# Performance work log

Measured on AMD Instinct MI355X. Metric: run time of the kernel, lower is better.

The kernel has to match this reference:

```python
import jax, jax.numpy as jnp
import numpy as np

_WINDOW = 2  # len_sort_window in the torch module


def _butterfly_indices(L, D):
    """Replicates get_butterfly_matrix's index columns.

    Column 0 is arange(L). Each subsequent column d (1-indexed) is arange(L)
    rolled right by shift_offset, where shift_offset starts at 0 and increases
    by 2 per column (mod L). The butterfly_factor_to_matrix result is computed
    but never used in the original code, so it is omitted here.
    Result[i, d] = (i - shift_d) mod L.
    """
    shifts = np.concatenate([[0], (_WINDOW * np.arange(D - 1)) % L])  # [D]
    idx = (np.arange(L)[:, None] - shifts[None, :]) % L  # [L, D]
    return jnp.asarray(idx, dtype=jnp.int32)


def setup_inputs() -> dict:
    key = jax.random.key(0)
    v = jax.random.normal(key, (16, 16384, 128), dtype=jnp.float32)
    return {"v": v}


def reference(v):
    B, L, D = v.shape  # static under jit
    idx = _butterfly_indices(L, D)  # [L, D]
    # v_shifted[b, i, d] = v[b, idx[i, d], d]  (torch.gather along dim 1)
    v_shifted = jnp.take_along_axis(v, jnp.broadcast_to(idx[None], (B, L, D)), axis=1)
    # window-2 ascending sort == compare-exchange (min, max)
    vw = v_shifted.reshape(B, L // _WINDOW, _WINDOW, D)
    lo = jnp.minimum(vw[:, :, 0], vw[:, :, 1])
    hi = jnp.maximum(vw[:, :, 0], vw[:, :, 1])
    out = jnp.stack([lo, hi], axis=2).reshape(B, L, D)
    return out
```

## Files before the change

kernel.cpp:

```cpp
#include <hip/hip_runtime.h>
#include <cstdint>
#include <cstddef>

#define L_DIM 16384
#define D_DIM 128
#define B_DIM 16

#define TR 256
#define DG 32
#define HALO 64
#define ROWS (TR + HALO)

__global__ __launch_bounds__(256) void butterfly_cmpex_kernel(
    const float* __restrict__ v, float* __restrict__ out) {
  __shared__ float lds[ROWS * DG];

  const int rtile = blockIdx.x;
  const int g     = blockIdx.y;
  const int b     = blockIdx.z;
  const int r0    = rtile * TR;
  const int d0    = g * DG;
  const int smax  = 64 * g + 60;
  const int rin0  = r0 - smax;

  const int t    = threadIdx.x;
  const int lane = t & 63;
  const int wave = t >> 6;

  const float* vb = v + (size_t)b * L_DIM * D_DIM;

  const int lrow  = lane >> 3;
  const int lcol4 = lane & 7;
  for (int chunk = wave; chunk < ROWS / 8; chunk += 4) {
    const int grow = (rin0 + chunk * 8 + lrow) & (L_DIM - 1);
    const float* gp = vb + (size_t)grow * D_DIM + d0 + lcol4 * 4;
    float* lp = &lds[chunk * 8 * DG];
    __builtin_amdgcn_global_load_lds(
        (const __attribute__((address_space(1))) uint32_t*)gp,
        (__attribute__((address_space(3))) uint32_t*)lp,
        16 , 0 , 0 );
  }
  __syncthreads();

  const int c  = t & 31;
  const int jg = t >> 5;
  const int d  = d0 + c;
  const int s  = (d == 0) ? 0 : (2 * d - 2);
  const int roff = smax - s;

  float* outb = out + (size_t)b * L_DIM * D_DIM;

#pragma unroll
  for (int k = 0; k < TR / 16; ++k) {
    const int j_local = k * 8 + jg;
    const int lr = 2 * j_local + roff;
    const float a0 = lds[lr * DG + c];
    const float a1 = lds[(lr + 1) * DG + c];
    const float lo = fminf(a0, a1);
    const float hi = fmaxf(a0, a1);
    const size_t o = (size_t)(r0 + 2 * j_local) * D_DIM + d;
    outb[o]         = lo;
    outb[o + D_DIM] = hi;
  }
}

extern "C" void kernel_launch(void* const* d_in, const int* in_sizes, int n_in,
                              void* d_out, int out_size, void* d_ws, size_t ws_size,
                              hipStream_t stream) {
  const float* v = (const float*)d_in[0];
  float* out = (float*)d_out;
  dim3 grid(L_DIM / TR, D_DIM / DG, B_DIM);
  dim3 block(256);
  butterfly_cmpex_kernel<<<grid, block, 0, stream>>>(v, out);
}
```

Before: 232.4 us.

## Stream long row chunks through an LDS ring buffer with async prefetch

Each block now processes a 2048-row chunk, streaming input into a 512-row LDS ring via async global-to-LDS loads issued two batches ahead with manual vmcnt waits. This cuts the halo re-read overhead of small tiles and overlaps loads with the compare-exchange and stores. It risks lower occupancy and parallelism due to fewer, larger blocks, and relies on careful waitcnt and barrier correctness for ring slot reuse.

```diff
diff --git a/kernel.cpp b/kernel.cpp
--- a/kernel.cpp
+++ b/kernel.cpp
@@ -6,62 +6,89 @@
 #define D_DIM 128
 #define B_DIM 16
 
-#define TR 256
 #define DG 32
-#define HALO 64
-#define ROWS (TR + HALO)
+#define NRING 512
+#define RMASK (NRING - 1)
+#define BATCH 128
+#define CHUNK 2048
+#define NB_OUT (CHUNK / BATCH)
 
-__global__ __launch_bounds__(256) void butterfly_cmpex_kernel(
+typedef const __attribute__((address_space(1))) uint32_t GBuf;
+typedef __attribute__((address_space(3))) uint32_t LBuf;
+
+__global__ __launch_bounds__(512, 4) void butterfly_ring_kernel(
     const float* __restrict__ v, float* __restrict__ out) {
-  __shared__ float lds[ROWS * DG];
+  __shared__ float lds[NRING * DG];
 
-  const int rtile = blockIdx.x;
+  const int chunk = blockIdx.x;
   const int g     = blockIdx.y;
   const int b     = blockIdx.z;
-  const int r0    = rtile * TR;
-  const int d0    = g * DG;
-  const int smax  = 64 * g + 60;
-  const int rin0  = r0 - smax;
+
+  const int R0  = chunk * CHUNK;
+  const int d0  = g * DG;
+  const int IN0 = R0 - 64 * (g + 1);
 
   const int t    = threadIdx.x;
   const int lane = t & 63;
   const int wave = t >> 6;
 
-  const float* vb = v + (size_t)b * L_DIM * D_DIM;
+  const float* vb = v   + (size_t)b * (L_DIM * D_DIM);
+  float*       ob = out + (size_t)b * (L_DIM * D_DIM);
 
   const int lrow  = lane >> 3;
   const int lcol4 = lane & 7;
-  for (int chunk = wave; chunk < ROWS / 8; chunk += 4) {
-    const int grow = (rin0 + chunk * 8 + lrow) & (L_DIM - 1);
-    const float* gp = vb + (size_t)grow * D_DIM + d0 + lcol4 * 4;
-    float* lp = &lds[chunk * 8 * DG];
-    __builtin_amdgcn_global_load_lds(
-        (const __attribute__((address_space(1))) uint32_t*)gp,
-        (__attribute__((address_space(3))) uint32_t*)lp,
-        16 , 0 , 0 );
+
+#define ISSUE_BATCH(kk)                                                      \
+  {                                                                          \
+    _Pragma("unroll")                                                        \
+    for (int p = 0; p < 2; ++p) {                                            \
+      const int sub  = wave * 2 + p;                              \
+      const int rb   = sub * 8 + lrow;                 \
+      const int grow = (IN0 + (kk)*BATCH + rb) & (L_DIM - 1);                \
+      const float* gp = vb + (size_t)grow * D_DIM + d0 + lcol4 * 4;          \
+      float* lp = &lds[((((kk)*BATCH) & RMASK) + sub * 8) * DG];             \
+      __builtin_amdgcn_global_load_lds((GBuf*)gp, (LBuf*)lp, 16, 0, 0);      \
+    }                                                                        \
   }
-  __syncthreads();
 
-  const int c  = t & 31;
-  const int jg = t >> 5;
-  const int d  = d0 + c;
-  const int s  = (d == 0) ? 0 : (2 * d - 2);
-  const int roff = smax - s;
+  const int c   = t & 31;
+  const int jr2 = (t >> 5) * 2;
+  const int d   = d0 + c;
+  const int boff = (d == 0) ? 64 : (66 - 2 * c);
 
-  float* outb = out + (size_t)b * L_DIM * D_DIM;
+  ISSUE_BATCH(0);
+  ISSUE_BATCH(1);
 
+#pragma unroll 4
+  for (int k = 0; k < NB_OUT; ++k) {
+    if (k < NB_OUT - 1) ISSUE_BATCH(k + 2);
+    if (k == 0) {
+      asm volatile("s_waitcnt vmcnt(2)" ::: "memory");
+    } else if (k < NB_OUT - 1) {
+      asm volatile("s_waitcnt vmcnt(10)" ::: "memory");
+    } else {
+      asm volatile("s_waitcnt vmcnt(8)" ::: "memory");
+    }
+    __builtin_amdgcn_s_barrier();
+
+    const int kb  = k * BATCH;
+    const int R0k = R0 + kb;
 #pragma unroll
-  for (int k = 0; k < TR / 16; ++k) {
-    const int j_local = k * 8 + jg;
-    const int lr = 2 * j_local + roff;
-    const float a0 = lds[lr * DG + c];
-    const float a1 = lds[(lr + 1) * DG + c];
-    const float lo = fminf(a0, a1);
-    const float hi = fmaxf(a0, a1);
-    const size_t o = (size_t)(r0 + 2 * j_local) * D_DIM + d;
-    outb[o]         = lo;
-    outb[o + D_DIM] = hi;
+    for (int q = 0; q < 4; ++q) {
+      const int m2  = 32 * q + jr2;
+      const int rel = kb + m2 + boff;
+      const int s0  = rel & RMASK;
+      const int s1  = (rel + 1) & RMASK;
+      const float a0 = lds[s0 * DG + c];
+      const float a1 = lds[s1 * DG + c];
+      const float lo = fminf(a0, a1);
+      const float hi = fmaxf(a0, a1);
+      float* op = ob + (size_t)(R0k + m2) * D_DIM + d;
+      op[0]     = lo;
+      op[D_DIM] = hi;
+    }
   }
+#undef ISSUE_BATCH
 }
 
 extern "C" void kernel_launch(void* const* d_in, const int* in_sizes, int n_in,
@@ -69,7 +96,7 @@
                               hipStream_t stream) {
   const float* v = (const float*)d_in[0];
   float* out = (float*)d_out;
-  dim3 grid(L_DIM / TR, D_DIM / DG, B_DIM);
-  dim3 block(256);
-  butterfly_cmpex_kernel<<<grid, block, 0, stream>>>(v, out);
+  dim3 grid(L_DIM / CHUNK, D_DIM / DG, B_DIM);
+  dim3 block(512);
+  butterfly_ring_kernel<<<grid, block, 0, stream>>>(v, out);
 }
```

Result: slower. 239.4 us (+3.0%).

## Stage tiles through registers with float4 loads and double row tile size

Applied to the files above, without the earlier changes.

Replaces the direct global-to-LDS async loads with float4 global loads into registers, which are then written to LDS. The row tile grows from 256 to 512 with 512-thread blocks, so the 64-row halo is a smaller fraction of each tile and redundant reads drop. The risks are higher register and LDS use per block, which may lower occupancy, and losing the hardware path that writes global loads straight into LDS.

```diff
diff --git a/kernel.cpp b/kernel.cpp
--- a/kernel.cpp
+++ b/kernel.cpp
@@ -6,12 +6,13 @@
 #define D_DIM 128
 #define B_DIM 16
 
-#define TR 256
+#define TR 512
 #define DG 32
 #define HALO 64
 #define ROWS (TR + HALO)
+#define NSWEEP (ROWS / 64)
 
-__global__ __launch_bounds__(256) void butterfly_cmpex_kernel(
+__global__ __launch_bounds__(512, 2) void butterfly_reg_kernel(
     const float* __restrict__ v, float* __restrict__ out) {
   __shared__ float lds[ROWS * DG];
 
@@ -23,44 +24,45 @@
   const int smax  = 64 * g + 60;
   const int rin0  = r0 - smax;
 
-  const int t    = threadIdx.x;
-  const int lane = t & 63;
-  const int wave = t >> 6;
+  const int t = threadIdx.x;
 
-  const float* vb = v + (size_t)b * L_DIM * D_DIM;
+  const float* vb = v   + (size_t)b * (L_DIM * D_DIM);
+  float*       ob = out + (size_t)b * (L_DIM * D_DIM);
 
-  const int lrow  = lane >> 3;
-  const int lcol4 = lane & 7;
-  for (int chunk = wave; chunk < ROWS / 8; chunk += 4) {
-    const int grow = (rin0 + chunk * 8 + lrow) & (L_DIM - 1);
-    const float* gp = vb + (size_t)grow * D_DIM + d0 + lcol4 * 4;
-    float* lp = &lds[chunk * 8 * DG];
-    __builtin_amdgcn_global_load_lds(
-        (const __attribute__((address_space(1))) uint32_t*)gp,
-        (__attribute__((address_space(3))) uint32_t*)lp,
-        16 , 0 , 0 );
+  const int srow  = t >> 3;
+  const int scol4 = t & 7;
+  float4 stg[NSWEEP];
+#pragma unroll
+  for (int s = 0; s < NSWEEP; ++s) {
+    const int rt   = s * 64 + srow;
+    const int grow = (rin0 + rt) & (L_DIM - 1);
+    stg[s] = *reinterpret_cast<const float4*>(
+        vb + (size_t)grow * D_DIM + d0 + scol4 * 4);
+  }
+#pragma unroll
+  for (int s = 0; s < NSWEEP; ++s) {
+    const int rt = s * 64 + srow;
+    *reinterpret_cast<float4*>(&lds[rt * DG + scol4 * 4]) = stg[s];
   }
   __syncthreads();
 
   const int c  = t & 31;
-  const int jg = t >> 5;
+  const int sg = t >> 5;
   const int d  = d0 + c;
-  const int s  = (d == 0) ? 0 : (2 * d - 2);
-  const int roff = smax - s;
-
-  float* outb = out + (size_t)b * L_DIM * D_DIM;
+  const int s_d  = (d == 0) ? 0 : (2 * d - 2);
+  const int boff = smax - s_d;
 
 #pragma unroll
-  for (int k = 0; k < TR / 16; ++k) {
-    const int j_local = k * 8 + jg;
-    const int lr = 2 * j_local + roff;
+  for (int kk = 0; kk < TR / 32; ++kk) {
+    const int pr = kk * 16 + sg;
+    const int lr = 2 * pr + boff;
     const float a0 = lds[lr * DG + c];
     const float a1 = lds[(lr + 1) * DG + c];
     const float lo = fminf(a0, a1);
     const float hi = fmaxf(a0, a1);
-    const size_t o = (size_t)(r0 + 2 * j_local) * D_DIM + d;
-    outb[o]         = lo;
-    outb[o + D_DIM] = hi;
+    float* op = ob + (size_t)(r0 + 2 * pr) * D_DIM + d;
+    op[0]     = lo;
+    op[D_DIM] = hi;
   }
 }
 
@@ -70,6 +72,6 @@
   const float* v = (const float*)d_in[0];
   float* out = (float*)d_out;
   dim3 grid(L_DIM / TR, D_DIM / DG, B_DIM);
-  dim3 block(256);
-  butterfly_cmpex_kernel<<<grid, block, 0, stream>>>(v, out);
+  dim3 block(512);
+  butterfly_reg_kernel<<<grid, block, 0, stream>>>(v, out);
 }
```

Result: no change. 229.4 us (-1.3%).
